# Kernel tuning notes

Measured on AMD Instinct MI355X. Metric: run time of the kernel, lower is better.

## Reference

```python
import jax, jax.numpy as jnp
import numpy as np

N_WEIGHTS = 16777216  # 2**24
BATCH = 16777216
PRIOR_SIGMA = 1.0
HALF_LOG_2PI = 0.9189385332046727  # 0.5 * log(2*pi)


def _normal_logprob(x, mu, sigma):
    # Gaussian log density, elementwise
    z = (x - mu) / sigma
    return -0.5 * z * z - jnp.log(sigma) - HALF_LOG_2PI


def setup_inputs() -> dict:
    key = jax.random.key(0)
    k1, k2, k3, k4, k5 = jax.random.split(key, 5)
    noisy_weights = jax.random.normal(k1, (N_WEIGHTS,), dtype=jnp.float32)
    mu_weights = jax.random.normal(k2, (N_WEIGHTS,), dtype=jnp.float32)
    # strictly positive sigmas in [0.5, 1.5)
    sigma_weights = jax.random.uniform(k3, (N_WEIGHTS,), dtype=jnp.float32) + 0.5
    mu_prediction = jax.random.normal(k4, (BATCH,), dtype=jnp.float32)
    sigma_prediction = jnp.float32(0.7)  # single scalar value
    y_true = jax.random.normal(k5, (BATCH,), dtype=jnp.float32)
    return {
        "noisy_weights": noisy_weights,
        "mu_weights": mu_weights,
        "sigma_weights": sigma_weights,
        "mu_prediction": mu_prediction,
        "sigma_prediction": sigma_prediction,
        "y_true": y_true,
    }


def reference(noisy_weights, mu_weights, sigma_weights, mu_prediction, sigma_prediction, y_true):
    # log p(w) under prior N(0, prior_sigma), summed
    loss_prior = _normal_logprob(noisy_weights, 0.0, jnp.float32(PRIOR_SIGMA)).sum()
    # log N(y_true | mu_prediction, sigma_prediction), summed over batch
    loss_likelihood = _normal_logprob(y_true, mu_prediction, sigma_prediction).sum()
    # log q(w | mu_weights, sigma_weights), summed over weights
    loss_variational = _normal_logprob(noisy_weights, mu_weights, sigma_weights).sum()
    # total = variational - prior - likelihood (negative ELBO)
    return loss_variational - loss_prior - loss_likelihood
```

## Files before the change

### kernel.cpp

```cpp
#include <hip/hip_runtime.h>


constexpr int BLOCKS  = 2048;
constexpr int THREADS = 256;
constexpr float LN2          = 0.6931471805599453f;
constexpr float HALF_LOG_2PI = 0.9189385332046727f;

__global__ __launch_bounds__(THREADS) void elbo_partial(
    const float* __restrict__ xw,
    const float* __restrict__ muw,
    const float* __restrict__ sgw,
    const float* __restrict__ mup,
    const float* __restrict__ sp_ptr,
    const float* __restrict__ yt,
    float* __restrict__ partial,
    int n4)
{
    const float4* x4 = (const float4*)xw;
    const float4* m4 = (const float4*)muw;
    const float4* s4 = (const float4*)sgw;
    const float4* p4 = (const float4*)mup;
    const float4* y4 = (const float4*)yt;

    float aw = 0.f;
    float al = 0.f;
    float ab = 0.f;
    int idx    = blockIdx.x * blockDim.x + threadIdx.x;
    int stride = gridDim.x * blockDim.x;
    for (int i = idx; i < n4; i += stride) {
        float4 xv = x4[i];
        float4 mv = m4[i];
        float4 sv = s4[i];
        float4 pv = p4[i];
        float4 yv = y4[i];
#define COMP(c) {                                   \
        float dx = xv.c - mv.c;                     \
        float r  = __builtin_amdgcn_rcpf(sv.c);     \
        float z  = dx * r;                          \
        aw += xv.c * xv.c - z * z;                  \
        al += __log2f(sv.c);                        \
        float d  = yv.c - pv.c;                     \
        ab += d * d; }
        COMP(x) COMP(y) COMP(z) COMP(w)
#undef COMP
    }
    float sp = sp_ptr[0];
    float inv2sp2 = 0.5f * __builtin_amdgcn_rcpf(sp * sp);
    float v = 0.5f * aw - LN2 * al + inv2sp2 * ab;

    for (int off = 32; off > 0; off >>= 1)
        v += __shfl_down(v, off);

    __shared__ float lds[THREADS / 64];
    int lane = threadIdx.x & 63;
    int wave = threadIdx.x >> 6;
    if (lane == 0) lds[wave] = v;
    __syncthreads();
    if (threadIdx.x == 0)
        partial[blockIdx.x] = lds[0] + lds[1] + lds[2] + lds[3];
}

__global__ __launch_bounds__(256) void elbo_final(
    const float* __restrict__ partial,
    const float* __restrict__ sp_ptr,
    float* __restrict__ out,
    int nblocks, float batch_f)
{
    float v = 0.f;
    for (int i = threadIdx.x; i < nblocks; i += 256)
        v += partial[i];
    for (int off = 32; off > 0; off >>= 1)
        v += __shfl_down(v, off);
    __shared__ float lds[4];
    int lane = threadIdx.x & 63;
    int wave = threadIdx.x >> 6;
    if (lane == 0) lds[wave] = v;
    __syncthreads();
    if (threadIdx.x == 0) {
        float sp = sp_ptr[0];
        float c  = batch_f * (logf(sp) + HALF_LOG_2PI);
        out[0] = lds[0] + lds[1] + lds[2] + lds[3] + c;
    }
}

extern "C" void kernel_launch(void* const* d_in, const int* in_sizes, int n_in,
                              void* d_out, int out_size, void* d_ws, size_t ws_size,
                              hipStream_t stream) {
    const float* xw  = (const float*)d_in[0];
    const float* muw = (const float*)d_in[1];
    const float* sgw = (const float*)d_in[2];
    const float* mup = (const float*)d_in[3];
    const float* sp  = (const float*)d_in[4];
    const float* yt  = (const float*)d_in[5];
    float* out     = (float*)d_out;
    float* partial = (float*)d_ws;

    int n  = in_sizes[0];
    int n4 = n / 4;

    elbo_partial<<<BLOCKS, THREADS, 0, stream>>>(xw, muw, sgw, mup, sp, yt,
                                                 partial, n4);
    elbo_final<<<1, 256, 0, stream>>>(partial, sp, out, BLOCKS,
                                      (float)in_sizes[5]);
}
```

Before: 300.3 us.

## Use fixed-work blocks with batched upfront loads instead of grid-stride loop

Measured after the change: 297.2 us. About the same (-1.0%).

```diff
diff --git a/kernel.cpp b/kernel.cpp
--- a/kernel.cpp
+++ b/kernel.cpp
@@ -1,12 +1,73 @@
 #include <hip/hip_runtime.h>
 
 
-constexpr int BLOCKS  = 2048;
 constexpr int THREADS = 256;
+constexpr int ITERS   = 4;
 constexpr float LN2          = 0.6931471805599453f;
 constexpr float HALF_LOG_2PI = 0.9189385332046727f;
 
-__global__ __launch_bounds__(THREADS) void elbo_partial(
+__global__ __launch_bounds__(THREADS, 4) void elbo_partial_fixed(
+    const float* __restrict__ xw,
+    const float* __restrict__ muw,
+    const float* __restrict__ sgw,
+    const float* __restrict__ mup,
+    const float* __restrict__ sp_ptr,
+    const float* __restrict__ yt,
+    float* __restrict__ partial)
+{
+    const float4* x4 = (const float4*)xw;
+    const float4* m4 = (const float4*)muw;
+    const float4* s4 = (const float4*)sgw;
+    const float4* p4 = (const float4*)mup;
+    const float4* y4 = (const float4*)yt;
+
+    const int base = blockIdx.x * (THREADS * ITERS) + threadIdx.x;
+
+    float4 xv[ITERS], mv[ITERS], sv[ITERS], pv[ITERS], yv[ITERS];
+#pragma unroll
+    for (int it = 0; it < ITERS; ++it) {
+        int i = base + it * THREADS;
+        xv[it] = x4[i];
+        mv[it] = m4[i];
+        sv[it] = s4[i];
+        pv[it] = p4[i];
+        yv[it] = y4[i];
+    }
+
+    float aw = 0.f;
+    float al = 0.f;
+    float ab = 0.f;
+#pragma unroll
+    for (int it = 0; it < ITERS; ++it) {
+#define COMP(c) {                                        \
+        float dx = xv[it].c - mv[it].c;                  \
+        float r  = __builtin_amdgcn_rcpf(sv[it].c);      \
+        float z  = dx * r;                               \
+        aw += xv[it].c * xv[it].c - z * z;               \
+        al += __log2f(sv[it].c);                         \
+        float d  = yv[it].c - pv[it].c;                  \
+        ab += d * d; }
+        COMP(x) COMP(y) COMP(z) COMP(w)
+#undef COMP
+    }
+
+    float sp = sp_ptr[0];
+    float inv2sp2 = 0.5f * __builtin_amdgcn_rcpf(sp * sp);
+    float v = 0.5f * aw - LN2 * al + inv2sp2 * ab;
+
+    for (int off = 32; off > 0; off >>= 1)
+        v += __shfl_down(v, off);
+
+    __shared__ float lds[THREADS / 64];
+    int lane = threadIdx.x & 63;
+    int wave = threadIdx.x >> 6;
+    if (lane == 0) lds[wave] = v;
+    __syncthreads();
+    if (threadIdx.x == 0)
+        partial[blockIdx.x] = lds[0] + lds[1] + lds[2] + lds[3];
+}
+
+__global__ __launch_bounds__(THREADS) void elbo_partial_generic(
     const float* __restrict__ xw,
     const float* __restrict__ muw,
     const float* __restrict__ sgw,
@@ -22,17 +83,11 @@
     const float4* p4 = (const float4*)mup;
     const float4* y4 = (const float4*)yt;
 
-    float aw = 0.f;
-    float al = 0.f;
-    float ab = 0.f;
+    float aw = 0.f, al = 0.f, ab = 0.f;
     int idx    = blockIdx.x * blockDim.x + threadIdx.x;
     int stride = gridDim.x * blockDim.x;
     for (int i = idx; i < n4; i += stride) {
-        float4 xv = x4[i];
-        float4 mv = m4[i];
-        float4 sv = s4[i];
-        float4 pv = p4[i];
-        float4 yv = y4[i];
+        float4 xv = x4[i], mv = m4[i], sv = s4[i], pv = p4[i], yv = y4[i];
 #define COMP(c) {                                   \
         float dx = xv.c - mv.c;                     \
         float r  = __builtin_amdgcn_rcpf(sv.c);     \
@@ -97,9 +152,18 @@
 
     int n  = in_sizes[0];
     int n4 = n / 4;
+    const int chunk = THREADS * ITERS;
 
-    elbo_partial<<<BLOCKS, THREADS, 0, stream>>>(xw, muw, sgw, mup, sp, yt,
-                                                 partial, n4);
-    elbo_final<<<1, 256, 0, stream>>>(partial, sp, out, BLOCKS,
+    int nblocks;
+    if (n4 % chunk == 0) {
+        nblocks = n4 / chunk;
+        elbo_partial_fixed<<<nblocks, THREADS, 0, stream>>>(
+            xw, muw, sgw, mup, sp, yt, partial);
+    } else {
+        nblocks = 2048;
+        elbo_partial_generic<<<nblocks, THREADS, 0, stream>>>(
+            xw, muw, sgw, mup, sp, yt, partial, n4);
+    }
+    elbo_final<<<1, 256, 0, stream>>>(partial, sp, out, nblocks,
                                       (float)in_sizes[5]);
 }
```
